# Kernel tuning notes

Hardware: AMD Instinct MI355X
Metric: run time of the kernel (lower is better)

## Reference

```python
import jax, jax.numpy as jnp
import numpy as np

SIGMA_DEG = 2.5
EPS = 1e-8


def setup_inputs() -> dict:
    key = jax.random.key(0)
    k1, k2 = jax.random.split(key)
    b, t, o = 4, 16, 32
    # trajectory points: lat in [-90, 90], lon in [-180, 180]
    lat_pts = jax.random.uniform(k1, (b, t, o, 1), jnp.float32, -90.0, 90.0)
    lon_pts = jax.random.uniform(k2, (b, t, o, 1), jnp.float32, -180.0, 180.0)
    traj = jnp.concatenate([lat_pts, lon_pts], axis=-1)  # (b, t, o, 2)
    lat = jnp.linspace(-90.0, 90.0, 181, dtype=jnp.float32)   # (h,)
    lon = jnp.linspace(-180.0, 180.0, 360, dtype=jnp.float32)  # (w,)
    return {"traj": traj, "lat": lat, "lon": lon}


def reference(traj, lat, lon):
    # traj: (b,t,o,2), lat: (h,), lon: (w,)
    inv_sigma2 = 1.0 / (SIGMA_DEG ** 2 + EPS)
    lat_t = traj[..., 0][:, :, :, None, None]  # (b,t,o,1,1)
    lon_t = traj[..., 1][:, :, :, None, None]
    d2 = ((lat[None, None, None, :, None] - lat_t) ** 2
          + (lon[None, None, None, None, :] - lon_t) ** 2) * inv_sigma2  # (b,t,o,h,w)
    heat = jnp.exp(-0.5 * d2).sum(axis=2)  # (b,t,h,w)
    heat = heat / (jnp.max(heat, axis=(-2, -1), keepdims=True) + EPS)
    return heat
```

## Files before the change

kernel.cpp:

```cpp
#include <hip/hip_runtime.h>


#define NH 181
#define NW 360
#define NO 32
#define NIMG 64
#define NCH 6
#define CROWS 32
#define TM 8
#define NTX 45
#define TY 4
#define NTHR 192

__device__ __forceinline__ float img_scale(const float* __restrict__ maxbuf, int img) {
    float m = 0.0f;
    #pragma unroll
    for (int c = 0; c < NCH; ++c) m = fmaxf(m, maxbuf[img * NCH + c]);
    return 1.0f / (m + 1e-8f);
}

template <bool WRITE>
__global__ __launch_bounds__(NTHR) void traj_pass(
    const float* __restrict__ traj,
    const float* __restrict__ lat,
    const float* __restrict__ lon,
    float* __restrict__ out,
    float* __restrict__ maxbuf
) {
    const int img = blockIdx.x;
    const int chunk = blockIdx.y;
    const int tid = threadIdx.x;

    __shared__ float fs[NO][CROWS];
    __shared__ float gs[NO][NW];
    __shared__ float red[NTHR / 64];

    const float C = -0.5f / (2.5f * 2.5f + 1e-8f);
    const float scale = WRITE ? img_scale(maxbuf, img) : 1.0f;

    for (int i = tid; i < NO * CROWS; i += NTHR) {
        const int k = i >> 5, r = i & 31;
        const int row = chunk * CROWS + r;
        float v = 0.0f;
        if (row < NH) {
            const float d = lat[row] - traj[(img * NO + k) * 2 + 0];
            v = __expf(C * d * d);
        }
        fs[k][r] = v;
    }
    for (int i = tid; i < NO * NW; i += NTHR) {
        const int k = i / NW, w = i - k * NW;
        const float d = lon[w] - traj[(img * NO + k) * 2 + 1];
        gs[k][w] = __expf(C * d * d) * scale;
    }
    __syncthreads();

    float lmax = 0.0f;
    if (tid < NTX * TY) {
        const int tx = tid % NTX, ty = tid / NTX;
        const int w0 = tx * 4;
        const int r0 = ty * TM;

        float acc[TM][8];
        #pragma unroll
        for (int i = 0; i < TM; ++i)
            #pragma unroll
            for (int j = 0; j < 8; ++j) acc[i][j] = 0.0f;

        #pragma unroll 2
        for (int k = 0; k < NO; ++k) {
            const float4 gA = *(const float4*)&gs[k][w0];
            const float4 gB = *(const float4*)&gs[k][w0 + 180];
            const float4 fA = *(const float4*)&fs[k][r0];
            const float4 fB = *(const float4*)&fs[k][r0 + 4];
            const float fr[TM] = {fA.x, fA.y, fA.z, fA.w, fB.x, fB.y, fB.z, fB.w};
            const float gr[8]  = {gA.x, gA.y, gA.z, gA.w, gB.x, gB.y, gB.z, gB.w};
            #pragma unroll
            for (int i = 0; i < TM; ++i)
                #pragma unroll
                for (int j = 0; j < 8; ++j)
                    acc[i][j] += fr[i] * gr[j];
        }

        if (WRITE) {
            float* __restrict__ op = out + (size_t)img * NH * NW;
            #pragma unroll
            for (int i = 0; i < TM; ++i) {
                const int r = chunk * CROWS + r0 + i;
                if (r < NH) {
                    const float4 vA = {acc[i][0], acc[i][1], acc[i][2], acc[i][3]};
                    const float4 vB = {acc[i][4], acc[i][5], acc[i][6], acc[i][7]};
                    *(float4*)&op[r * NW + w0] = vA;
                    *(float4*)&op[r * NW + w0 + 180] = vB;
                }
            }
        } else {
            #pragma unroll
            for (int i = 0; i < TM; ++i) {
                const int r = chunk * CROWS + r0 + i;
                if (r < NH) {
                    #pragma unroll
                    for (int j = 0; j < 8; ++j) lmax = fmaxf(lmax, acc[i][j]);
                }
            }
        }
    }

    if (!WRITE) {
        #pragma unroll
        for (int off = 32; off > 0; off >>= 1)
            lmax = fmaxf(lmax, __shfl_down(lmax, off, 64));
        if ((tid & 63) == 0) red[tid >> 6] = lmax;
        __syncthreads();
        if (tid == 0)
            maxbuf[img * NCH + chunk] = fmaxf(fmaxf(red[0], red[1]), red[2]);
    }
}

extern "C" void kernel_launch(void* const* d_in, const int* in_sizes, int n_in,
                              void* d_out, int out_size, void* d_ws, size_t ws_size,
                              hipStream_t stream) {
    const float* traj = (const float*)d_in[0];
    const float* lat  = (const float*)d_in[1];
    const float* lon  = (const float*)d_in[2];
    float* out = (float*)d_out;
    float* maxbuf = (float*)d_ws;

    dim3 grid(NIMG, NCH);
    traj_pass<false><<<grid, NTHR, 0, stream>>>(traj, lat, lon, out, maxbuf);
    traj_pass<true><<<grid, NTHR, 0, stream>>>(traj, lat, lon, out, maxbuf);
}
```

Baseline: 90.01 us.

## Fuse max and write passes into one cooperative kernel with grid sync

```diff
diff --git a/kernel.cpp b/kernel.cpp
--- a/kernel.cpp
+++ b/kernel.cpp
@@ -1,4 +1,7 @@
 #include <hip/hip_runtime.h>
+#include <hip/hip_cooperative_groups.h>
+
+namespace cg = cooperative_groups;
 
 
 #define NH 181
@@ -11,6 +14,113 @@
 #define NTX 45
 #define TY 4
 #define NTHR 192
+
+#define SIGC (-0.5f / (2.5f * 2.5f + 1e-8f))
+
+
+__global__ __launch_bounds__(NTHR) void traj_fused(
+    const float* __restrict__ traj,
+    const float* __restrict__ lat,
+    const float* __restrict__ lon,
+    float* __restrict__ out,
+    float* __restrict__ maxbuf
+) {
+    const int img = blockIdx.x;
+    const int chunk = blockIdx.y;
+    const int tid = threadIdx.x;
+
+    __shared__ float fs[NO][CROWS];
+    __shared__ float gs[NO][NW];
+    __shared__ float red[NTHR / 64];
+
+    for (int i = tid; i < NO * CROWS; i += NTHR) {
+        const int k = i >> 5, r = i & 31;
+        const int row = chunk * CROWS + r;
+        float v = 0.0f;
+        if (row < NH) {
+            const float d = lat[row] - traj[(img * NO + k) * 2 + 0];
+            v = __expf(SIGC * d * d);
+        }
+        fs[k][r] = v;
+    }
+    for (int i = tid; i < NO * NW; i += NTHR) {
+        const int k = i / NW, w = i - k * NW;
+        const float d = lon[w] - traj[(img * NO + k) * 2 + 1];
+        gs[k][w] = __expf(SIGC * d * d);
+    }
+    __syncthreads();
+
+    const int tx = tid % NTX, ty = tid / NTX;
+    const int w0 = tx * 4;
+    const int r0 = ty * TM;
+    const bool active = tid < NTX * TY;
+
+    float acc[TM][8];
+    #pragma unroll
+    for (int i = 0; i < TM; ++i)
+        #pragma unroll
+        for (int j = 0; j < 8; ++j) acc[i][j] = 0.0f;
+
+    float lmax = 0.0f;
+    if (active) {
+        #pragma unroll 2
+        for (int k = 0; k < NO; ++k) {
+            const float4 gA = *(const float4*)&gs[k][w0];
+            const float4 gB = *(const float4*)&gs[k][w0 + 180];
+            const float4 fA = *(const float4*)&fs[k][r0];
+            const float4 fB = *(const float4*)&fs[k][r0 + 4];
+            const float fr[TM] = {fA.x, fA.y, fA.z, fA.w, fB.x, fB.y, fB.z, fB.w};
+            const float gr[8]  = {gA.x, gA.y, gA.z, gA.w, gB.x, gB.y, gB.z, gB.w};
+            #pragma unroll
+            for (int i = 0; i < TM; ++i)
+                #pragma unroll
+                for (int j = 0; j < 8; ++j)
+                    acc[i][j] += fr[i] * gr[j];
+        }
+        #pragma unroll
+        for (int i = 0; i < TM; ++i) {
+            if (chunk * CROWS + r0 + i < NH) {
+                #pragma unroll
+                for (int j = 0; j < 8; ++j) lmax = fmaxf(lmax, acc[i][j]);
+            }
+        }
+    }
+
+    #pragma unroll
+    for (int off = 32; off > 0; off >>= 1)
+        lmax = fmaxf(lmax, __shfl_down(lmax, off, 64));
+    if ((tid & 63) == 0) red[tid >> 6] = lmax;
+    __syncthreads();
+    if (tid == 0) {
+        const float bm = fmaxf(fmaxf(red[0], red[1]), red[2]);
+        __hip_atomic_store(&maxbuf[img * NCH + chunk], bm,
+                           __ATOMIC_RELEASE, __HIP_MEMORY_SCOPE_AGENT);
+    }
+
+    cg::this_grid().sync();
+
+    float m = 0.0f;
+    #pragma unroll
+    for (int c = 0; c < NCH; ++c)
+        m = fmaxf(m, __hip_atomic_load(&maxbuf[img * NCH + c],
+                                       __ATOMIC_ACQUIRE, __HIP_MEMORY_SCOPE_AGENT));
+    const float s = 1.0f / (m + 1e-8f);
+
+    if (active) {
+        float* __restrict__ op = out + (size_t)img * NH * NW;
+        #pragma unroll
+        for (int i = 0; i < TM; ++i) {
+            const int r = chunk * CROWS + r0 + i;
+            if (r < NH) {
+                const float4 vA = {acc[i][0] * s, acc[i][1] * s, acc[i][2] * s, acc[i][3] * s};
+                const float4 vB = {acc[i][4] * s, acc[i][5] * s, acc[i][6] * s, acc[i][7] * s};
+                *(float4*)&op[r * NW + w0] = vA;
+                *(float4*)&op[r * NW + w0 + 180] = vB;
+            }
+        }
+    }
+}
+
 
 __device__ __forceinline__ float img_scale(const float* __restrict__ maxbuf, int img) {
     float m = 0.0f;
@@ -35,7 +145,6 @@
     __shared__ float gs[NO][NW];
     __shared__ float red[NTHR / 64];
 
-    const float C = -0.5f / (2.5f * 2.5f + 1e-8f);
     const float scale = WRITE ? img_scale(maxbuf, img) : 1.0f;
 
     for (int i = tid; i < NO * CROWS; i += NTHR) {
@@ -44,14 +153,14 @@
         float v = 0.0f;
         if (row < NH) {
             const float d = lat[row] - traj[(img * NO + k) * 2 + 0];
-            v = __expf(C * d * d);
+            v = __expf(SIGC * d * d);
         }
         fs[k][r] = v;
     }
     for (int i = tid; i < NO * NW; i += NTHR) {
         const int k = i / NW, w = i - k * NW;
         const float d = lon[w] - traj[(img * NO + k) * 2 + 1];
-        gs[k][w] = __expf(C * d * d) * scale;
+        gs[k][w] = __expf(SIGC * d * d) * scale;
     }
     __syncthreads();
 
@@ -97,8 +206,7 @@
         } else {
             #pragma unroll
             for (int i = 0; i < TM; ++i) {
-                const int r = chunk * CROWS + r0 + i;
-                if (r < NH) {
+                if (chunk * CROWS + r0 + i < NH) {
                     #pragma unroll
                     for (int j = 0; j < 8; ++j) lmax = fmaxf(lmax, acc[i][j]);
                 }
@@ -126,7 +234,13 @@
     float* out = (float*)d_out;
     float* maxbuf = (float*)d_ws;
 
-    dim3 grid(NIMG, NCH);
-    traj_pass<false><<<grid, NTHR, 0, stream>>>(traj, lat, lon, out, maxbuf);
-    traj_pass<true><<<grid, NTHR, 0, stream>>>(traj, lat, lon, out, maxbuf);
-}
+    void* args[] = { (void*)&traj, (void*)&lat, (void*)&lon, (void*)&out, (void*)&maxbuf };
+    hipError_t err = hipLaunchCooperativeKernel(
+        (const void*)traj_fused, dim3(NIMG, NCH), dim3(NTHR), args, 0, stream);
+
+    if (err != hipSuccess) {
+        dim3 grid(NIMG, NCH);
+        traj_pass<false><<<grid, NTHR, 0, stream>>>(traj, lat, lon, out, maxbuf);
+        traj_pass<true><<<grid, NTHR, 0, stream>>>(traj, lat, lon, out, maxbuf);
+    }
+}
```

After: 180.9 us. 2.01x slower.
